# Optimization experiments

Measured on AMD Instinct MI355X. Metric: run time of the kernel, lower is better.

Reference implementation:

```python
import jax, jax.numpy as jnp
import numpy as np

P, F, FR = 288, 7, 12      # time slots per day, days per week, sampling frequency scale
CHEB_K = 2
HID = 64


def _ste(time_index, SE, W_se, b_se, T_tod, T_dow):
    """Spatio-temporal embedding: learned spatial embedding projected to et_dim,
    plus time-of-day and day-of-week temporal embeddings. -> [B, N, et]"""
    t = time_index * FR
    tod = T_tod[t % P]                 # [B, et]
    dow = T_dow[(t // P) % F]          # [B, et]
    se = SE @ W_se + b_se              # [N, et]
    return se[None, :, :] + (tod + dow)[:, None, :]


def _avwgcn(x, STE, R, SC, Wpool, bpool):
    """Adaptive-vertex-weight graph conv (AGCRN-style) with dynamic STE-driven
    adjacency blended with dynamic relation R and static correlation SC.
    x: [B,N,Cin], STE: [B,N,et], R: [B,N,N], SC: [N,N]."""
    A = jax.nn.softmax(
        jax.nn.relu(jnp.einsum('bnd,bmd->bnm', STE, STE)) + R + SC[None], axis=-1)
    # Chebyshev polynomial supports applied to x (T0 = I handled implicitly)
    xs = [x, jnp.einsum('bnm,bmc->bnc', A, x)]
    for _ in range(CHEB_K - 2):
        xs.append(2.0 * jnp.einsum('bnm,bmc->bnc', A, xs[-1]) - xs[-2])
    x_g = jnp.stack(xs, axis=2)                        # [B,N,K,Cin]
    # per-node adaptive weights: W_n = STE @ Wpool; contracted without
    # materializing the [B,N,K,Cin,Cout] tensor
    g = jnp.einsum('bnki,dkio->bndo', x_g, Wpool)      # [B,N,et,Cout]
    out = jnp.einsum('bndo,bnd->bno', g, STE) + jnp.einsum('bnd,do->bno', STE, bpool)
    return out


def setup_inputs() -> dict:
    key = jax.random.key(0)
    ks = jax.random.split(key, 12)
    B, N, Din, et, es = 32, 1024, 1, 16, 16
    std = 0.1
    return {
        "x": jax.random.normal(ks[0], (B, N, Din), jnp.float32),
        "R": jax.random.normal(ks[1], (B, N, N), jnp.float32) * std,
        "state": jax.random.normal(ks[2], (B, N, HID), jnp.float32),
        "SC": jax.random.normal(ks[3], (N, N), jnp.float32) * std,
        "SE": jax.random.normal(ks[4], (N, es), jnp.float32),
        "W_se": jax.random.normal(ks[5], (es, et), jnp.float32) * std,
        "b_se": jnp.zeros((et,), jnp.float32),
        "T_tod": jax.random.normal(ks[6], (P, et), jnp.float32) * std,
        "T_dow": jax.random.normal(ks[7], (F, et), jnp.float32) * std,
        "W_gate": jax.random.normal(ks[8], (et, CHEB_K, Din + HID, 2 * HID), jnp.float32) * std,
        "b_gate": jnp.zeros((et, 2 * HID), jnp.float32),
        "W_upd": jax.random.normal(ks[9], (et, CHEB_K, Din + HID, HID), jnp.float32) * std,
        "b_upd": jnp.zeros((et, HID), jnp.float32),
        "time_index": jax.random.randint(ks[10], (B,), 0, P * F),
    }


def reference(x, R, state, SC, SE, W_se, b_se, T_tod, T_dow,
              W_gate, b_gate, W_upd, b_upd, time_index):
    STE = _ste(time_index, SE, W_se, b_se, T_tod, T_dow)       # [B,N,et]
    ins = jnp.concatenate([x, state], axis=-1)                 # [B,N,Din+H]
    z_r = jax.nn.sigmoid(_avwgcn(ins, STE, R, SC, W_gate, b_gate))
    z, r = jnp.split(z_r, 2, axis=-1)                          # each [B,N,H]
    cand = jnp.concatenate([x, z * state], axis=-1)
    hc = jnp.tanh(_avwgcn(cand, STE, R, SC, W_upd, b_upd))
    return r * state + (1.0 - r) * hc                          # [B,N,H]
```

## Files before the change

kernel.cpp:

```cpp
#include <hip/hip_runtime.h>
#include <math.h>

namespace {
constexpr int BB = 32;
constexpr int NN = 1024;
constexpr int ET = 16;
constexpr int HH = 64;
constexpr int CIN = 65;
constexpr int KI = 2*CIN;
constexpr int COG = 2*HH;
constexpr int COU = HH;
constexpr int PP = 288;
constexpr int FF = 7;
constexpr int FRQ = 12;
constexpr int XK = 160;
constexpr int KP = 168;

typedef __attribute__((ext_vector_type(4))) float f32x4;
typedef __attribute__((ext_vector_type(8))) short s16x8;
typedef unsigned long long ull;

__device__ __forceinline__ float bf2f(unsigned short u) {
    unsigned v = ((unsigned)u) << 16;
    return __builtin_bit_cast(float, v);
}
__device__ __forceinline__ unsigned short f2bf(float f) {
    unsigned u = __builtin_bit_cast(unsigned, f);
    u += 0x7fffu + ((u >> 16) & 1u);
    return (unsigned short)(u >> 16);
}

__global__ void k_prep1(const float* __restrict__ SE, const float* __restrict__ Wse,
                        const float* __restrict__ bse, const float* __restrict__ Ttod,
                        const float* __restrict__ Tdow, const int* __restrict__ tidx,
                        float* __restrict__ se, float* __restrict__ tt) {
    int idx = blockIdx.x*blockDim.x + threadIdx.x;
    if (idx < NN*ET) {
        int n = idx / ET, d = idx % ET;
        float acc = bse[d];
        #pragma unroll
        for (int e = 0; e < ET; ++e) acc += SE[n*ET + e]*Wse[e*ET + d];
        se[idx] = acc;
    } else if (idx < NN*ET + BB*ET) {
        int r = idx - NN*ET;
        int b = r / ET, d = r % ET;
        int t = tidx[b]*FRQ;
        tt[r] = Ttod[(t % PP)*ET + d] + Tdow[((t/PP) % FF)*ET + d];
    }
}

__global__ void k_prep2bf(const float* __restrict__ se, const float* __restrict__ tt,
                          unsigned short* __restrict__ stebf) {
    int idx = blockIdx.x*blockDim.x + threadIdx.x;
    if (idx >= BB*NN*ET) return;
    int d = idx % ET;
    int n = (idx/ET) % NN;
    int b = idx/(ET*NN);
    stebf[idx] = f2bf(se[n*ET+d] + tt[b*ET+d]);
}

__global__ void k_prep3bt(const float* __restrict__ tt, const float* __restrict__ Wg,
                          const float* __restrict__ Wu,
                          unsigned short* __restrict__ Wbtg, unsigned short* __restrict__ Wbtu) {
    int idx = blockIdx.x*blockDim.x + threadIdx.x;
    constexpr int NG = BB*KP*COG;
    constexpr int NU = BB*KP*COU;
    if (idx < NG) {
        int b = idx/(KP*COG); int r = idx%(KP*COG); int ki = r/COG; int o = r%COG;
        float v = 0.f;
        if (ki < KI) {
            #pragma unroll
            for (int d = 0; d < ET; ++d) v += tt[b*ET+d]*Wg[(d*KI + ki)*COG + o];
        }
        Wbtg[((size_t)b*COG + o)*KP + ki] = f2bf(v);
    } else if (idx < NG + NU) {
        int j = idx - NG;
        int b = j/(KP*COU); int r = j%(KP*COU); int ki = r/COU; int o = r%COU;
        float v = 0.f;
        if (ki < KI) {
            #pragma unroll
            for (int d = 0; d < ET; ++d) v += tt[b*ET+d]*Wu[(d*KI + ki)*COU + o];
        }
        Wbtu[((size_t)b*COU + o)*KP + ki] = f2bf(v);
    }
}

__global__ void k_pack(const float* __restrict__ x, const float* __restrict__ sv,
                       const float* __restrict__ axx, const float* __restrict__ ax2,
                       unsigned short* __restrict__ xgbf) {
    int idx = blockIdx.x*blockDim.x + threadIdx.x;
    if (idx >= BB*NN*(XK/2)) return;
    int row = idx/(XK/2), c = idx%(XK/2);
    float v[2];
    #pragma unroll
    for (int h = 0; h < 2; ++h) {
        int k = 2*c + h;
        float val;
        if (k == 0) val = x[row];
        else if (k < CIN) val = sv[(size_t)row*HH + k - 1];
        else if (k == CIN) val = axx[row];
        else if (k < KI) val = ax2[(size_t)row*HH + k - CIN - 1];
        else val = 0.f;
        v[h] = val;
    }
    ((unsigned*)xgbf)[idx] = ((unsigned)f2bf(v[1]) << 16) | f2bf(v[0]);
}

__global__ void k_cvtVt(const float* __restrict__ V, unsigned short* __restrict__ vt) {
    int idx = blockIdx.x*blockDim.x + threadIdx.x;
    if (idx >= BB*128*64) return;
    int och = idx & 63, mb = (idx >> 6) & 127, b = idx >> 13;
    const float* src = V + ((size_t)b*NN + mb*8)*HH + och;
    float v0=src[0], v1=src[HH], v2=src[2*HH], v3=src[3*HH];
    float v4=src[4*HH], v5=src[5*HH], v6=src[6*HH], v7=src[7*HH];
    ull lo = (ull)f2bf(v0) | ((ull)f2bf(v1)<<16) | ((ull)f2bf(v2)<<32) | ((ull)f2bf(v3)<<48);
    ull hi = (ull)f2bf(v4) | ((ull)f2bf(v5)<<16) | ((ull)f2bf(v6)<<32) | ((ull)f2bf(v7)<<48);
    ull* dst = (ull*)(vt + (size_t)idx*8);
    dst[0] = lo; dst[1] = hi;
}

constexpr int SSTR   = 1048;
constexpr int S_OFF  = 0;
constexpr int XV_OFF = 33536;
constexpr int MSH_OFF  = 37632;
constexpr int MSHC_OFF = 37888;
constexpr int LP_OFF   = 37952;
constexpr int AXP_OFF  = 38208;
constexpr int LSH_OFF  = 38464;
constexpr int SMEM_BYTES = 38528;

template<int PASS>
__global__ __launch_bounds__(256, 4) void k_attn(
    const unsigned short* __restrict__ stebf, const float* __restrict__ Rg,
    const float* __restrict__ SCg, const float* __restrict__ xg,
    const unsigned short* __restrict__ vt,
    float* __restrict__ Mr, float* __restrict__ Li, float* __restrict__ Axx,
    float* __restrict__ outp)
{
    extern __shared__ char smem[];
    const int t = threadIdx.x, lane = t & 63, w = t >> 6;
    const int c15 = lane & 15, g = lane >> 4;
    const int strip = blockIdx.x, b = blockIdx.y;
    const size_t bN = (size_t)b * NN;
    const int r0 = strip * 16;

    float* Mshf  = (float*)(smem + MSH_OFF);
    float* MshCf = (float*)(smem + MSHC_OFF);
    float* Lpf   = (float*)(smem + LP_OFF);
    float* Axpf  = (float*)(smem + AXP_OFF);
    float* Lshf  = (float*)(smem + LSH_OFF);

    if (PASS == 1) {
        ((float4*)(smem + XV_OFF))[t] = ((const float4*)(xg + bN))[t];
    }

    {
        s16x8 af = {0,0,0,0,0,0,0,0};
        if (g < 2) af = *(const s16x8*)(stebf + (bN + r0 + c15)*ET + g*8);
        const float* Rb  = Rg  + (bN + r0 + g*4)*NN;
        const float* SCb = SCg + (size_t)(r0 + g*4)*NN;
        float mx0 = -INFINITY, mx1 = -INFINITY, mx2 = -INFINITY, mx3 = -INFINITY;
        float rc[4], scv[4];
        {
            int col = w*16 + c15;
            #pragma unroll
            for (int q = 0; q < 4; ++q) { rc[q] = Rb[(size_t)q*NN + col]; scv[q] = SCb[(size_t)q*NN + col]; }
        }
        for (int j = 0; j < 16; ++j) {
            int colB = j*64 + w*16 + c15;
            s16x8 bf = {0,0,0,0,0,0,0,0};
            if (g < 2) bf = *(const s16x8*)(stebf + (bN + colB)*ET + g*8);
            float rn[4] = {0.f,0.f,0.f,0.f}, sn[4] = {0.f,0.f,0.f,0.f};
            if (j < 15) {
                int col = colB + 64;
                #pragma unroll
                for (int q = 0; q < 4; ++q) { rn[q] = Rb[(size_t)q*NN + col]; sn[q] = SCb[(size_t)q*NN + col]; }
            }
            f32x4 zero = {0.f,0.f,0.f,0.f};
            f32x4 d = __builtin_amdgcn_mfma_f32_16x16x32_bf16(af, bf, zero, 0, 0, 0);
            #pragma unroll
            for (int q = 0; q < 4; ++q) {
                float s = fmaxf(d[q], 0.f) + rc[q] + scv[q];
                if (PASS == 1) {
                    if (q == 0) mx0 = fmaxf(mx0, s);
                    if (q == 1) mx1 = fmaxf(mx1, s);
                    if (q == 2) mx2 = fmaxf(mx2, s);
                    if (q == 3) mx3 = fmaxf(mx3, s);
                }
                int rowl = g*4 + q;
                *(unsigned short*)(smem + S_OFF + (unsigned)(rowl*SSTR + colB)*2u) = f2bf(s);
            }
            #pragma unroll
            for (int q = 0; q < 4; ++q) { rc[q] = rn[q]; scv[q] = sn[q]; }
        }
        if (PASS == 1) {
            float mxa[4] = {mx0, mx1, mx2, mx3};
            #pragma unroll
            for (int q = 0; q < 4; ++q) {
                float m = mxa[q];
                m = fmaxf(m, __shfl_xor(m, 1));
                m = fmaxf(m, __shfl_xor(m, 2));
                m = fmaxf(m, __shfl_xor(m, 4));
                m = fmaxf(m, __shfl_xor(m, 8));
                if (c15 == 0) Mshf[w*16 + g*4 + q] = m;
            }
        }
    }
    __syncthreads();

    if (PASS == 1) {
        if (t < 16) {
            float m = fmaxf(fmaxf(Mshf[t], Mshf[16+t]), fmaxf(Mshf[32+t], Mshf[48+t]));
            MshCf[t] = m;
            Mr[bN + r0 + t] = m;
        }
    } else {
        if (t < 16) MshCf[t] = Mr[bN + r0 + t];
        if (t >= 64 && t < 80) Lshf[t-64] = Li[bN + r0 + (t-64)];
    }
    __syncthreads();

    {
        const int rowl = c15;
        const float m = MshCf[rowl];
        float L = 0.f, ax = 0.f;
        for (int it = 0; it < 16; ++it) {
            int k = w*256 + it*16 + g*4;
            unsigned byteo = (unsigned)(rowl*SSTR + k)*2u;
            ull v = *(ull*)(smem + S_OFF + byteo);
            float s0 = bf2f((unsigned short)v);
            float s1 = bf2f((unsigned short)(v >> 16));
            float s2 = bf2f((unsigned short)(v >> 32));
            float s3 = bf2f((unsigned short)(v >> 48));
            float p0 = __expf(s0 - m), p1 = __expf(s1 - m);
            float p2 = __expf(s2 - m), p3 = __expf(s3 - m);
            if (PASS == 1) {
                float4 xq = *(const float4*)(smem + XV_OFF + k*4);
                L += (p0 + p1) + (p2 + p3);
                ax += p0*xq.x + p1*xq.y + p2*xq.z + p3*xq.w;
            }
            unsigned lo = ((unsigned)f2bf(p1) << 16) | f2bf(p0);
            unsigned hi = ((unsigned)f2bf(p3) << 16) | f2bf(p2);
            *(ull*)(smem + S_OFF + byteo) = ((ull)hi << 32) | lo;
        }
        if (PASS == 1) {
            L += __shfl_xor(L, 16); L += __shfl_xor(L, 32);
            ax += __shfl_xor(ax, 16); ax += __shfl_xor(ax, 32);
            if (g == 0) { Lpf[w*16 + rowl] = L; Axpf[w*16 + rowl] = ax; }
        }
    }
    __syncthreads();
    if (PASS == 1) {
        if (t < 16) {
            float Lt = Lpf[t] + Lpf[16+t] + Lpf[32+t] + Lpf[48+t];
            float li = 1.f / Lt;
            Lshf[t] = li;
            Li[bN + r0 + t] = li;
            Axx[bN + r0 + t] = (Axpf[t] + Axpf[16+t] + Axpf[32+t] + Axpf[48+t]) * li;
        }
        __syncthreads();
    }

    {
        f32x4 acc = {0.f,0.f,0.f,0.f};
        const unsigned short* vtb = vt + ((size_t)b*128*64 + (w*16 + c15))*8;
        #pragma unroll 4
        for (int j = 0; j < 16; ++j) {
            #pragma unroll
            for (int ks = 0; ks < 2; ++ks) {
                s16x8 a  = *(const s16x8*)(smem + S_OFF + (unsigned)(c15*SSTR + j*64 + ks*32 + g*8)*2u);
                s16x8 bv = *(const s16x8*)(vtb + (size_t)(j*8 + ks*4 + g)*512);
                acc = __builtin_amdgcn_mfma_f32_16x16x32_bf16(a, bv, acc, 0, 0, 0);
            }
        }
        #pragma unroll
        for (int q = 0; q < 4; ++q) {
            int rowl = g*4 + q;
            float li = Lshf[rowl];
            outp[(bN + r0 + rowl)*HH + w*16 + c15] = acc[q] * li;
        }
    }
}

template<int COUT>
__global__ __launch_bounds__(256, 2) void k_bapplyM(
    const unsigned short* __restrict__ Wbt, const float* __restrict__ bias,
    const float* __restrict__ tt, const unsigned short* __restrict__ xgbf,
    float* __restrict__ partial)
{
    constexpr int NTP = COUT/64;
    __shared__ __align__(16) unsigned short Wl[COUT*KP];
    const int t = threadIdx.x, lane = t & 63, w = t >> 6;
    const int c15 = lane & 15, g = lane >> 4;
    const int b = blockIdx.y, n0 = blockIdx.x*64;

    {
        const unsigned* src = (const unsigned*)(Wbt + (size_t)b*COUT*KP);
        unsigned* dst = (unsigned*)Wl;
        #pragma unroll
        for (int e = t; e < COUT*KP/2; e += 256) dst[e] = src[e];
    }
    __syncthreads();

    f32x4 acc[4][NTP];
    #pragma unroll
    for (int mt = 0; mt < 4; ++mt)
        #pragma unroll
        for (int nt = 0; nt < NTP; ++nt) acc[mt][nt] = (f32x4){0.f,0.f,0.f,0.f};

    for (int ks = 0; ks < 5; ++ks) {
        s16x8 a[4];
        #pragma unroll
        for (int mt = 0; mt < 4; ++mt)
            a[mt] = *(const s16x8*)(xgbf + ((size_t)b*NN + n0 + mt*16 + c15)*XK + ks*32 + g*8);
        #pragma unroll
        for (int nt = 0; nt < NTP; ++nt) {
            int o = (w*NTP + nt)*16 + c15;
            s16x8 bf = *(const s16x8*)(Wl + o*KP + ks*32 + g*8);
            #pragma unroll
            for (int mt = 0; mt < 4; ++mt)
                acc[mt][nt] = __builtin_amdgcn_mfma_f32_16x16x32_bf16(a[mt], bf, acc[mt][nt], 0, 0, 0);
        }
    }

    #pragma unroll
    for (int nt = 0; nt < NTP; ++nt) {
        int o = (w*NTP + nt)*16 + c15;
        float bo = 0.f;
        #pragma unroll
        for (int d = 0; d < ET; ++d) bo += tt[b*ET+d]*bias[d*COUT+o];
        #pragma unroll
        for (int mt = 0; mt < 4; ++mt)
            #pragma unroll
            for (int q = 0; q < 4; ++q)
                partial[((size_t)b*NN + n0 + mt*16 + g*4 + q)*COUT + o] = acc[mt][nt][q] + bo;
    }
}

__global__ __launch_bounds__(256, 2) void k_napplyM_gate(
    const float* __restrict__ se_g, const float* __restrict__ Wg,
    const float* __restrict__ bias, const unsigned short* __restrict__ xgbf,
    const float* __restrict__ partial, const float* __restrict__ state,
    float* __restrict__ zs, float* __restrict__ rout)
{
    __shared__ __align__(16) unsigned short Wnt[COG*KP];
    __shared__ float se_l[ET];
    const int t = threadIdx.x, lane = t & 63, w = t >> 6;
    const int c15 = lane & 15, g = lane >> 4;
    const int n = blockIdx.x;
    if (t < ET) se_l[t] = se_g[n*ET + t];
    __syncthreads();

    for (int e = t; e < COG*KP; e += 256) {
        int ki = e/COG, o = e%COG;
        float v = 0.f;
        if (ki < KI) {
            #pragma unroll
            for (int d = 0; d < ET; ++d) v += se_l[d]*Wg[(d*KI + ki)*COG + o];
        }
        Wnt[o*KP + ki] = f2bf(v);
    }
    __syncthreads();

    f32x4 acc[2][2];
    #pragma unroll
    for (int mt = 0; mt < 2; ++mt)
        #pragma unroll
        for (int nt = 0; nt < 2; ++nt) acc[mt][nt] = (f32x4){0.f,0.f,0.f,0.f};

    for (int ks = 0; ks < 5; ++ks) {
        s16x8 a[2];
        #pragma unroll
        for (int mt = 0; mt < 2; ++mt)
            a[mt] = *(const s16x8*)(xgbf + ((size_t)(mt*16 + c15)*NN + n)*XK + ks*32 + g*8);
        #pragma unroll
        for (int nt = 0; nt < 2; ++nt) {
            int o = (w*2 + nt)*16 + c15;
            s16x8 bf = *(const s16x8*)(Wnt + o*KP + ks*32 + g*8);
            #pragma unroll
            for (int mt = 0; mt < 2; ++mt)
                acc[mt][nt] = __builtin_amdgcn_mfma_f32_16x16x32_bf16(a[mt], bf, acc[mt][nt], 0, 0, 0);
        }
    }

    #pragma unroll
    for (int nt = 0; nt < 2; ++nt) {
        int o = (w*2 + nt)*16 + c15;
        float bo = 0.f;
        #pragma unroll
        for (int d = 0; d < ET; ++d) bo += se_l[d]*bias[d*COG + o];
        #pragma unroll
        for (int mt = 0; mt < 2; ++mt)
            #pragma unroll
            for (int q = 0; q < 4; ++q) {
                int b = mt*16 + g*4 + q;
                size_t bn = (size_t)b*NN + n;
                float v = acc[mt][nt][q] + bo + partial[bn*COG + o];
                float gv = 1.f/(1.f + __expf(-v));
                if (o < HH) zs[bn*HH + o] = gv * state[bn*HH + o];
                else rout[bn*HH + o - HH] = gv;
            }
    }
}

__global__ __launch_bounds__(256, 2) void k_napplyM_upd(
    const float* __restrict__ se_g, const float* __restrict__ Wu,
    const float* __restrict__ bias, const unsigned short* __restrict__ xgbf,
    const float* __restrict__ partial, const float* __restrict__ rin,
    const float* __restrict__ state, float* __restrict__ out)
{
    __shared__ __align__(16) unsigned short Wnt[COU*KP];
    __shared__ float se_l[ET];
    const int t = threadIdx.x, lane = t & 63, w = t >> 6;
    const int c15 = lane & 15, g = lane >> 4;
    const int n = blockIdx.x;
    if (t < ET) se_l[t] = se_g[n*ET + t];
    __syncthreads();

    for (int e = t; e < COU*KP; e += 256) {
        int ki = e/COU, o = e%COU;
        float v = 0.f;
        if (ki < KI) {
            #pragma unroll
            for (int d = 0; d < ET; ++d) v += se_l[d]*Wu[(d*KI + ki)*COU + o];
        }
        Wnt[o*KP + ki] = f2bf(v);
    }
    __syncthreads();

    f32x4 acc[2];
    acc[0] = (f32x4){0.f,0.f,0.f,0.f};
    acc[1] = (f32x4){0.f,0.f,0.f,0.f};

    for (int ks = 0; ks < 5; ++ks) {
        s16x8 a[2];
        #pragma unroll
        for (int mt = 0; mt < 2; ++mt)
            a[mt] = *(const s16x8*)(xgbf + ((size_t)(mt*16 + c15)*NN + n)*XK + ks*32 + g*8);
        int o = w*16 + c15;
        s16x8 bf = *(const s16x8*)(Wnt + o*KP + ks*32 + g*8);
        #pragma unroll
        for (int mt = 0; mt < 2; ++mt)
            acc[mt] = __builtin_amdgcn_mfma_f32_16x16x32_bf16(a[mt], bf, acc[mt], 0, 0, 0);
    }

    {
        int o = w*16 + c15;
        float bo = 0.f;
        #pragma unroll
        for (int d = 0; d < ET; ++d) bo += se_l[d]*bias[d*COU + o];
        #pragma unroll
        for (int mt = 0; mt < 2; ++mt)
            #pragma unroll
            for (int q = 0; q < 4; ++q) {
                int b = mt*16 + g*4 + q;
                size_t bn = (size_t)b*NN + n;
                float v = acc[mt][q] + bo + partial[bn*COU + o];
                float hc = tanhf(v);
                float rv = rin[bn*HH + o];
                out[bn*HH + o] = rv*state[bn*HH + o] + (1.f - rv)*hc;
            }
    }
}

}

extern "C" void kernel_launch(void* const* d_in, const int* in_sizes, int n_in,
                              void* d_out, int out_size, void* d_ws, size_t ws_size,
                              hipStream_t stream) {
    const float* x     = (const float*)d_in[0];
    const float* R     = (const float*)d_in[1];
    const float* state = (const float*)d_in[2];
    const float* SC    = (const float*)d_in[3];
    const float* SE    = (const float*)d_in[4];
    const float* W_se  = (const float*)d_in[5];
    const float* b_se  = (const float*)d_in[6];
    const float* T_tod = (const float*)d_in[7];
    const float* T_dow = (const float*)d_in[8];
    const float* W_g   = (const float*)d_in[9];
    const float* b_g   = (const float*)d_in[10];
    const float* W_u   = (const float*)d_in[11];
    const float* b_u   = (const float*)d_in[12];
    const int*   tidx  = (const int*)d_in[13];
    float* out = (float*)d_out;
    float* ws = (float*)d_ws;

    float* se    = ws;
    float* tt    = se + 16384;
    float* Mr    = tt + 512;
    float* Li    = Mr + 32768;
    float* axx   = Li + 32768;
    float* axgs  = axx + 32768;
    float* zs    = axgs + 2097152;
    float* rr    = zs + 2097152;
    float* pg    = rr + 2097152;
    unsigned short* stebf = (unsigned short*)(pg + 4194304);
    unsigned short* Wbtg  = stebf + 524288;
    unsigned short* Wbtu  = Wbtg + 688128;
    unsigned short* xgbf  = Wbtu + 344064;
    unsigned short* vt    = xgbf + 5242880;
    float* axcs = axgs;
    float* pu   = pg;

    k_prep1<<<66, 256, 0, stream>>>(SE, W_se, b_se, T_tod, T_dow, tidx, se, tt);
    k_prep2bf<<<2048, 256, 0, stream>>>(se, tt, stebf);
    k_prep3bt<<<4032, 256, 0, stream>>>(tt, W_g, W_u, Wbtg, Wbtu);

    k_cvtVt<<<1024, 256, 0, stream>>>(state, vt);
    k_attn<1><<<dim3(64, 32), 256, SMEM_BYTES, stream>>>(
        stebf, R, SC, x, vt, Mr, Li, axx, axgs);
    k_pack<<<10240, 256, 0, stream>>>(x, state, axx, axgs, xgbf);
    k_bapplyM<COG><<<dim3(16, 32), 256, 0, stream>>>(Wbtg, b_g, tt, xgbf, pg);
    k_napplyM_gate<<<1024, 256, 0, stream>>>(se, W_g, b_g, xgbf, pg, state, zs, rr);

    k_cvtVt<<<1024, 256, 0, stream>>>(zs, vt);
    k_attn<2><<<dim3(64, 32), 256, SMEM_BYTES, stream>>>(
        stebf, R, SC, x, vt, Mr, Li, axx, axcs);
    k_pack<<<10240, 256, 0, stream>>>(x, zs, axx, axcs, xgbf);
    k_bapplyM<COU><<<dim3(16, 32), 256, 0, stream>>>(Wbtu, b_u, tt, xgbf, pu);
    k_napplyM_upd<<<1024, 256, 0, stream>>>(se, W_u, b_u, xgbf, pu, rr, state, out);
}
```

Measured before the change: 268.2 us.

## Contract adaptive weights per embedding dim in one MFMA apply kernel

Replaces the split batch-term/node-term apply kernels (which rebuilt per-node weight matrices in shared memory for every node) with a single kernel. It computes x_g·Wpool[d] for all 16 embedding dims via MFMA and contracts with the full STE in the epilogue. The attention kernel now writes its aggregated outputs directly as bf16 into the packed xg buffer, and gate outputs z*state and r are stored in bf16, removing the separate fp32 intermediates and pack copies. In exchange it does 16× more MFMA work per output, keeps 32 accumulators per lane (register pressure), and adds bf16 rounding to STE in the epilogue and to intermediate activations.

```diff
diff --git a/kernel.cpp b/kernel.cpp
--- a/kernel.cpp
+++ b/kernel.cpp
@@ -14,7 +14,6 @@
 constexpr int FF = 7;
 constexpr int FRQ = 12;
 constexpr int XK = 160;
-constexpr int KP = 168;
 
 typedef __attribute__((ext_vector_type(4))) float f32x4;
 typedef __attribute__((ext_vector_type(8))) short s16x8;
@@ -29,6 +28,8 @@
     u += 0x7fffu + ((u >> 16) & 1u);
     return (unsigned short)(u >> 16);
 }
+__device__ __forceinline__ float ldany(const float* p) { return *p; }
+__device__ __forceinline__ float ldany(const unsigned short* p) { return bf2f(*p); }
 
 __global__ void k_prep1(const float* __restrict__ SE, const float* __restrict__ Wse,
                         const float* __restrict__ bse, const float* __restrict__ Ttod,
@@ -59,60 +60,49 @@
     stebf[idx] = f2bf(se[n*ET+d] + tt[b*ET+d]);
 }
 
-__global__ void k_prep3bt(const float* __restrict__ tt, const float* __restrict__ Wg,
-                          const float* __restrict__ Wu,
-                          unsigned short* __restrict__ Wbtg, unsigned short* __restrict__ Wbtu) {
-    int idx = blockIdx.x*blockDim.x + threadIdx.x;
-    constexpr int NG = BB*KP*COG;
-    constexpr int NU = BB*KP*COU;
-    if (idx < NG) {
-        int b = idx/(KP*COG); int r = idx%(KP*COG); int ki = r/COG; int o = r%COG;
-        float v = 0.f;
-        if (ki < KI) {
-            #pragma unroll
-            for (int d = 0; d < ET; ++d) v += tt[b*ET+d]*Wg[(d*KI + ki)*COG + o];
-        }
-        Wbtg[((size_t)b*COG + o)*KP + ki] = f2bf(v);
-    } else if (idx < NG + NU) {
-        int j = idx - NG;
-        int b = j/(KP*COU); int r = j%(KP*COU); int ki = r/COU; int o = r%COU;
-        float v = 0.f;
-        if (ki < KI) {
-            #pragma unroll
-            for (int d = 0; d < ET; ++d) v += tt[b*ET+d]*Wu[(d*KI + ki)*COU + o];
-        }
-        Wbtu[((size_t)b*COU + o)*KP + ki] = f2bf(v);
-    }
-}
-
-__global__ void k_pack(const float* __restrict__ x, const float* __restrict__ sv,
-                       const float* __restrict__ axx, const float* __restrict__ ax2,
+__global__ void k_prepWpt(const float* __restrict__ Wg, const float* __restrict__ Wu,
+                          unsigned short* __restrict__ Wptg, unsigned short* __restrict__ Wptu) {
+    int idx = blockIdx.x*blockDim.x + threadIdx.x;
+    constexpr int NG2 = ET*COG*XK;
+    constexpr int NU2 = ET*COU*XK;
+    if (idx < NG2) {
+        int d = idx/(COG*XK), r = idx%(COG*XK), o = r/XK, ki = r%XK;
+        float v = (ki < KI) ? Wg[((size_t)d*KI + ki)*COG + o] : 0.f;
+        Wptg[((size_t)d*COG + o)*XK + ki] = f2bf(v);
+    } else if (idx < NG2 + NU2) {
+        int j = idx - NG2;
+        int d = j/(COU*XK), r = j%(COU*XK), o = r/XK, ki = r%XK;
+        float v = (ki < KI) ? Wu[((size_t)d*KI + ki)*COU + o] : 0.f;
+        Wptu[((size_t)d*COU + o)*XK + ki] = f2bf(v);
+    }
+}
+
+template<typename T>
+__global__ void k_pack(const float* __restrict__ x, const T* __restrict__ sv,
                        unsigned short* __restrict__ xgbf) {
     int idx = blockIdx.x*blockDim.x + threadIdx.x;
     if (idx >= BB*NN*(XK/2)) return;
     int row = idx/(XK/2), c = idx%(XK/2);
-    float v[2];
-    #pragma unroll
-    for (int h = 0; h < 2; ++h) {
-        int k = 2*c + h;
-        float val;
-        if (k == 0) val = x[row];
-        else if (k < CIN) val = sv[(size_t)row*HH + k - 1];
-        else if (k == CIN) val = axx[row];
-        else if (k < KI) val = ax2[(size_t)row*HH + k - CIN - 1];
-        else val = 0.f;
-        v[h] = val;
-    }
-    ((unsigned*)xgbf)[idx] = ((unsigned)f2bf(v[1]) << 16) | f2bf(v[0]);
-}
-
-__global__ void k_cvtVt(const float* __restrict__ V, unsigned short* __restrict__ vt) {
+    if (c < 32) {
+        int k0 = 2*c;
+        float v0 = (k0 == 0) ? x[row] : ldany(sv + (size_t)row*HH + k0 - 1);
+        float v1 = ldany(sv + (size_t)row*HH + k0);
+        ((unsigned*)xgbf)[(size_t)row*(XK/2) + c] = ((unsigned)f2bf(v1) << 16) | f2bf(v0);
+    } else if (c == 32) {
+        xgbf[(size_t)row*XK + 64] = f2bf(ldany(sv + (size_t)row*HH + 63));
+    } else if (c >= 65) {
+        ((unsigned*)xgbf)[(size_t)row*(XK/2) + c] = 0;
+    }
+}
+
+template<typename T>
+__global__ void k_cvtVt(const T* __restrict__ V, unsigned short* __restrict__ vt) {
     int idx = blockIdx.x*blockDim.x + threadIdx.x;
     if (idx >= BB*128*64) return;
     int och = idx & 63, mb = (idx >> 6) & 127, b = idx >> 13;
-    const float* src = V + ((size_t)b*NN + mb*8)*HH + och;
-    float v0=src[0], v1=src[HH], v2=src[2*HH], v3=src[3*HH];
-    float v4=src[4*HH], v5=src[5*HH], v6=src[6*HH], v7=src[7*HH];
+    const T* src = V + ((size_t)b*NN + mb*8)*HH + och;
+    float v0=ldany(src), v1=ldany(src+HH), v2=ldany(src+2*HH), v3=ldany(src+3*HH);
+    float v4=ldany(src+4*HH), v5=ldany(src+5*HH), v6=ldany(src+6*HH), v7=ldany(src+7*HH);
     ull lo = (ull)f2bf(v0) | ((ull)f2bf(v1)<<16) | ((ull)f2bf(v2)<<32) | ((ull)f2bf(v3)<<48);
     ull hi = (ull)f2bf(v4) | ((ull)f2bf(v5)<<16) | ((ull)f2bf(v6)<<32) | ((ull)f2bf(v7)<<48);
     ull* dst = (ull*)(vt + (size_t)idx*8);
@@ -134,8 +124,8 @@
     const unsigned short* __restrict__ stebf, const float* __restrict__ Rg,
     const float* __restrict__ SCg, const float* __restrict__ xg,
     const unsigned short* __restrict__ vt,
-    float* __restrict__ Mr, float* __restrict__ Li, float* __restrict__ Axx,
-    float* __restrict__ outp)
+    float* __restrict__ Mr, float* __restrict__ Li,
+    unsigned short* __restrict__ xgout)
 {
     extern __shared__ char smem[];
     const int t = threadIdx.x, lane = t & 63, w = t >> 6;
@@ -256,7 +246,8 @@
             float li = 1.f / Lt;
             Lshf[t] = li;
             Li[bN + r0 + t] = li;
-            Axx[bN + r0 + t] = (Axpf[t] + Axpf[16+t] + Axpf[32+t] + Axpf[48+t]) * li;
+            xgout[(bN + r0 + t)*XK + 65] =
+                f2bf((Axpf[t] + Axpf[16+t] + Axpf[32+t] + Axpf[48+t]) * li);
         }
         __syncthreads();
     }
@@ -277,189 +268,79 @@
         for (int q = 0; q < 4; ++q) {
             int rowl = g*4 + q;
             float li = Lshf[rowl];
-            outp[(bN + r0 + rowl)*HH + w*16 + c15] = acc[q] * li;
-        }
-    }
-}
-
-template<int COUT>
-__global__ __launch_bounds__(256, 2) void k_bapplyM(
-    const unsigned short* __restrict__ Wbt, const float* __restrict__ bias,
-    const float* __restrict__ tt, const unsigned short* __restrict__ xgbf,
-    float* __restrict__ partial)
+            xgout[(bN + r0 + rowl)*XK + 66 + w*16 + c15] = f2bf(acc[q] * li);
+        }
+    }
+}
+
+template<int COUT, int EPI>
+__global__ __launch_bounds__(256, 2) void k_apply(
+    const unsigned short* __restrict__ Wpt, const float* __restrict__ bias,
+    const unsigned short* __restrict__ stebf, const unsigned short* __restrict__ xgbf,
+    const float* __restrict__ state, unsigned short* __restrict__ zsbf,
+    unsigned short* __restrict__ rrbf, float* __restrict__ out)
 {
-    constexpr int NTP = COUT/64;
-    __shared__ __align__(16) unsigned short Wl[COUT*KP];
     const int t = threadIdx.x, lane = t & 63, w = t >> 6;
     const int c15 = lane & 15, g = lane >> 4;
-    const int b = blockIdx.y, n0 = blockIdx.x*64;
-
-    {
-        const unsigned* src = (const unsigned*)(Wbt + (size_t)b*COUT*KP);
-        unsigned* dst = (unsigned*)Wl;
+    const int n0 = blockIdx.x*32, b = blockIdx.y, oh = blockIdx.z;
+    const int o = oh*64 + w*16 + c15;
+
+    f32x4 acc[16][2];
+    #pragma unroll
+    for (int d = 0; d < 16; ++d) {
+        acc[d][0] = (f32x4){0.f,0.f,0.f,0.f};
+        acc[d][1] = (f32x4){0.f,0.f,0.f,0.f};
+    }
+
+    const unsigned short* Ar0 = xgbf + ((size_t)b*NN + n0 + c15)*XK + g*8;
+    const unsigned short* Ar1 = Ar0 + (size_t)16*XK;
+    const unsigned short* Bp  = Wpt + (size_t)o*XK + g*8;
+
+    for (int ks = 0; ks < 5; ++ks) {
+        s16x8 a0 = *(const s16x8*)(Ar0 + ks*32);
+        s16x8 a1 = *(const s16x8*)(Ar1 + ks*32);
         #pragma unroll
-        for (int e = t; e < COUT*KP/2; e += 256) dst[e] = src[e];
-    }
-    __syncthreads();
-
-    f32x4 acc[4][NTP];
+        for (int d = 0; d < 16; ++d) {
+            s16x8 bf = *(const s16x8*)(Bp + (size_t)d*COUT*XK + ks*32);
+            acc[d][0] = __builtin_amdgcn_mfma_f32_16x16x32_bf16(a0, bf, acc[d][0], 0, 0, 0);
+            acc[d][1] = __builtin_amdgcn_mfma_f32_16x16x32_bf16(a1, bf, acc[d][1], 0, 0, 0);
+        }
+    }
+
+    float biasv[16];
     #pragma unroll
-    for (int mt = 0; mt < 4; ++mt)
+    for (int d = 0; d < 16; ++d) biasv[d] = bias[d*COUT + o];
+
+    #pragma unroll
+    for (int mt = 0; mt < 2; ++mt) {
         #pragma unroll
-        for (int nt = 0; nt < NTP; ++nt) acc[mt][nt] = (f32x4){0.f,0.f,0.f,0.f};
-
-    for (int ks = 0; ks < 5; ++ks) {
-        s16x8 a[4];
-        #pragma unroll
-        for (int mt = 0; mt < 4; ++mt)
-            a[mt] = *(const s16x8*)(xgbf + ((size_t)b*NN + n0 + mt*16 + c15)*XK + ks*32 + g*8);
-        #pragma unroll
-        for (int nt = 0; nt < NTP; ++nt) {
-            int o = (w*NTP + nt)*16 + c15;
-            s16x8 bf = *(const s16x8*)(Wl + o*KP + ks*32 + g*8);
-            #pragma unroll
-            for (int mt = 0; mt < 4; ++mt)
-                acc[mt][nt] = __builtin_amdgcn_mfma_f32_16x16x32_bf16(a[mt], bf, acc[mt][nt], 0, 0, 0);
-        }
-    }
-
-    #pragma unroll
-    for (int nt = 0; nt < NTP; ++nt) {
-        int o = (w*NTP + nt)*16 + c15;
-        float bo = 0.f;
-        #pragma unroll
-        for (int d = 0; d < ET; ++d) bo += tt[b*ET+d]*bias[d*COUT+o];
-        #pragma unroll
-        for (int mt = 0; mt < 4; ++mt)
-            #pragma unroll
-            for (int q = 0; q < 4; ++q)
-                partial[((size_t)b*NN + n0 + mt*16 + g*4 + q)*COUT + o] = acc[mt][nt][q] + bo;
-    }
-}
-
-__global__ __launch_bounds__(256, 2) void k_napplyM_gate(
-    const float* __restrict__ se_g, const float* __restrict__ Wg,
-    const float* __restrict__ bias, const unsigned short* __restrict__ xgbf,
-    const float* __restrict__ partial, const float* __restrict__ state,
-    float* __restrict__ zs, float* __restrict__ rout)
-{
-    __shared__ __align__(16) unsigned short Wnt[COG*KP];
-    __shared__ float se_l[ET];
-    const int t = threadIdx.x, lane = t & 63, w = t >> 6;
-    const int c15 = lane & 15, g = lane >> 4;
-    const int n = blockIdx.x;
-    if (t < ET) se_l[t] = se_g[n*ET + t];
-    __syncthreads();
-
-    for (int e = t; e < COG*KP; e += 256) {
-        int ki = e/COG, o = e%COG;
-        float v = 0.f;
-        if (ki < KI) {
-            #pragma unroll
-            for (int d = 0; d < ET; ++d) v += se_l[d]*Wg[(d*KI + ki)*COG + o];
-        }
-        Wnt[o*KP + ki] = f2bf(v);
-    }
-    __syncthreads();
-
-    f32x4 acc[2][2];
-    #pragma unroll
-    for (int mt = 0; mt < 2; ++mt)
-        #pragma unroll
-        for (int nt = 0; nt < 2; ++nt) acc[mt][nt] = (f32x4){0.f,0.f,0.f,0.f};
-
-    for (int ks = 0; ks < 5; ++ks) {
-        s16x8 a[2];
-        #pragma unroll
-        for (int mt = 0; mt < 2; ++mt)
-            a[mt] = *(const s16x8*)(xgbf + ((size_t)(mt*16 + c15)*NN + n)*XK + ks*32 + g*8);
-        #pragma unroll
-        for (int nt = 0; nt < 2; ++nt) {
-            int o = (w*2 + nt)*16 + c15;
-            s16x8 bf = *(const s16x8*)(Wnt + o*KP + ks*32 + g*8);
-            #pragma unroll
-            for (int mt = 0; mt < 2; ++mt)
-                acc[mt][nt] = __builtin_amdgcn_mfma_f32_16x16x32_bf16(a[mt], bf, acc[mt][nt], 0, 0, 0);
-        }
-    }
-
-    #pragma unroll
-    for (int nt = 0; nt < 2; ++nt) {
-        int o = (w*2 + nt)*16 + c15;
-        float bo = 0.f;
-        #pragma unroll
-        for (int d = 0; d < ET; ++d) bo += se_l[d]*bias[d*COG + o];
-        #pragma unroll
-        for (int mt = 0; mt < 2; ++mt)
-            #pragma unroll
-            for (int q = 0; q < 4; ++q) {
-                int b = mt*16 + g*4 + q;
-                size_t bn = (size_t)b*NN + n;
-                float v = acc[mt][nt][q] + bo + partial[bn*COG + o];
-                float gv = 1.f/(1.f + __expf(-v));
-                if (o < HH) zs[bn*HH + o] = gv * state[bn*HH + o];
-                else rout[bn*HH + o - HH] = gv;
-            }
-    }
-}
-
-__global__ __launch_bounds__(256, 2) void k_napplyM_upd(
-    const float* __restrict__ se_g, const float* __restrict__ Wu,
-    const float* __restrict__ bias, const unsigned short* __restrict__ xgbf,
-    const float* __restrict__ partial, const float* __restrict__ rin,
-    const float* __restrict__ state, float* __restrict__ out)
-{
-    __shared__ __align__(16) unsigned short Wnt[COU*KP];
-    __shared__ float se_l[ET];
-    const int t = threadIdx.x, lane = t & 63, w = t >> 6;
-    const int c15 = lane & 15, g = lane >> 4;
-    const int n = blockIdx.x;
-    if (t < ET) se_l[t] = se_g[n*ET + t];
-    __syncthreads();
-
-    for (int e = t; e < COU*KP; e += 256) {
-        int ki = e/COU, o = e%COU;
-        float v = 0.f;
-        if (ki < KI) {
-            #pragma unroll
-            for (int d = 0; d < ET; ++d) v += se_l[d]*Wu[(d*KI + ki)*COU + o];
-        }
-        Wnt[o*KP + ki] = f2bf(v);
-    }
-    __syncthreads();
-
-    f32x4 acc[2];
-    acc[0] = (f32x4){0.f,0.f,0.f,0.f};
-    acc[1] = (f32x4){0.f,0.f,0.f,0.f};
-
-    for (int ks = 0; ks < 5; ++ks) {
-        s16x8 a[2];
-        #pragma unroll
-        for (int mt = 0; mt < 2; ++mt)
-            a[mt] = *(const s16x8*)(xgbf + ((size_t)(mt*16 + c15)*NN + n)*XK + ks*32 + g*8);
-        int o = w*16 + c15;
-        s16x8 bf = *(const s16x8*)(Wnt + o*KP + ks*32 + g*8);
-        #pragma unroll
-        for (int mt = 0; mt < 2; ++mt)
-            acc[mt] = __builtin_amdgcn_mfma_f32_16x16x32_bf16(a[mt], bf, acc[mt], 0, 0, 0);
-    }
-
-    {
-        int o = w*16 + c15;
-        float bo = 0.f;
-        #pragma unroll
-        for (int d = 0; d < ET; ++d) bo += se_l[d]*bias[d*COU + o];
-        #pragma unroll
-        for (int mt = 0; mt < 2; ++mt)
-            #pragma unroll
-            for (int q = 0; q < 4; ++q) {
-                int b = mt*16 + g*4 + q;
-                size_t bn = (size_t)b*NN + n;
-                float v = acc[mt][q] + bo + partial[bn*COU + o];
-                float hc = tanhf(v);
-                float rv = rin[bn*HH + o];
+        for (int q = 0; q < 4; ++q) {
+            int n = n0 + mt*16 + g*4 + q;
+            size_t bn = (size_t)b*NN + n;
+            const ull* sp = (const ull*)(stebf + bn*ET);
+            float val = 0.f;
+            #pragma unroll
+            for (int dd = 0; dd < 4; ++dd) {
+                ull sv4 = sp[dd];
+                float s0 = bf2f((unsigned short)sv4);
+                float s1 = bf2f((unsigned short)(sv4 >> 16));
+                float s2 = bf2f((unsigned short)(sv4 >> 32));
+                float s3 = bf2f((unsigned short)(sv4 >> 48));
+                val += s0*(acc[dd*4+0][mt][q] + biasv[dd*4+0]);
+                val += s1*(acc[dd*4+1][mt][q] + biasv[dd*4+1]);
+                val += s2*(acc[dd*4+2][mt][q] + biasv[dd*4+2]);
+                val += s3*(acc[dd*4+3][mt][q] + biasv[dd*4+3]);
+            }
+            if (EPI == 0) {
+                float gv = 1.f/(1.f + __expf(-val));
+                if (oh == 0) zsbf[bn*HH + o] = f2bf(gv * state[bn*HH + o]);
+                else         rrbf[bn*HH + (o - 64)] = f2bf(gv);
+            } else {
+                float hc = tanhf(val);
+                float rv = bf2f(rrbf[bn*HH + o]);
                 out[bn*HH + o] = rv*state[bn*HH + o] + (1.f - rv)*hc;
             }
+        }
     }
 }
 
@@ -485,38 +366,33 @@
     float* out = (float*)d_out;
     float* ws = (float*)d_ws;
 
-    float* se    = ws;
-    float* tt    = se + 16384;
-    float* Mr    = tt + 512;
-    float* Li    = Mr + 32768;
-    float* axx   = Li + 32768;
-    float* axgs  = axx + 32768;
-    float* zs    = axgs + 2097152;
-    float* rr    = zs + 2097152;
-    float* pg    = rr + 2097152;
-    unsigned short* stebf = (unsigned short*)(pg + 4194304);
-    unsigned short* Wbtg  = stebf + 524288;
-    unsigned short* Wbtu  = Wbtg + 688128;
-    unsigned short* xgbf  = Wbtu + 344064;
-    unsigned short* vt    = xgbf + 5242880;
-    float* axcs = axgs;
-    float* pu   = pg;
+    float* se = ws;
+    float* tt = se + 16384;
+    float* Mr = tt + 512;
+    float* Li = Mr + 32768;
+    unsigned short* stebf = (unsigned short*)(Li + 32768);
+    unsigned short* xgbf  = stebf + 524288;
+    unsigned short* zsbf  = xgbf + 5242880;
+    unsigned short* rrbf  = zsbf + 2097152;
+    unsigned short* vt    = rrbf + 2097152;
+    unsigned short* Wptg  = vt + 2097152;
+    unsigned short* Wptu  = Wptg + 327680;
 
     k_prep1<<<66, 256, 0, stream>>>(SE, W_se, b_se, T_tod, T_dow, tidx, se, tt);
     k_prep2bf<<<2048, 256, 0, stream>>>(se, tt, stebf);
-    k_prep3bt<<<4032, 256, 0, stream>>>(tt, W_g, W_u, Wbtg, Wbtu);
-
-    k_cvtVt<<<1024, 256, 0, stream>>>(state, vt);
+    k_prepWpt<<<1920, 256, 0, stream>>>(W_g, W_u, Wptg, Wptu);
+
+    k_cvtVt<float><<<1024, 256, 0, stream>>>(state, vt);
     k_attn<1><<<dim3(64, 32), 256, SMEM_BYTES, stream>>>(
-        stebf, R, SC, x, vt, Mr, Li, axx, axgs);
-    k_pack<<<10240, 256, 0, stream>>>(x, state, axx, axgs, xgbf);
-    k_bapplyM<COG><<<dim3(16, 32), 256, 0, stream>>>(Wbtg, b_g, tt, xgbf, pg);
-    k_napplyM_gate<<<1024, 256, 0, stream>>>(se, W_g, b_g, xgbf, pg, state, zs, rr);
-
-    k_cvtVt<<<1024, 256, 0, stream>>>(zs, vt);
+        stebf, R, SC, x, vt, Mr, Li, xgbf);
+    k_pack<float><<<10240, 256, 0, stream>>>(x, state, xgbf);
+    k_apply<COG, 0><<<dim3(32, 32, 2), 256, 0, stream>>>(
+        Wptg, b_g, stebf, xgbf, state, zsbf, rrbf, nullptr);
+
+    k_cvtVt<unsigned short><<<1024, 256, 0, stream>>>(zsbf, vt);
     k_attn<2><<<dim3(64, 32), 256, SMEM_BYTES, stream>>>(
-        stebf, R, SC, x, vt, Mr, Li, axx, axcs);
-    k_pack<<<10240, 256, 0, stream>>>(x, zs, axx, axcs, xgbf);
-    k_bapplyM<COU><<<dim3(16, 32), 256, 0, stream>>>(Wbtu, b_u, tt, xgbf, pu);
-    k_napplyM_upd<<<1024, 256, 0, stream>>>(se, W_u, b_u, xgbf, pu, rr, state, out);
-}
+        stebf, R, SC, x, vt, Mr, Li, xgbf);
+    k_pack<unsigned short><<<10240, 256, 0, stream>>>(x, zsbf, xgbf);
+    k_apply<COU, 1><<<dim3(32, 32, 1), 256, 0, stream>>>(
+        Wptu, b_u, stebf, xgbf, state, zsbf, rrbf, out);
+}
```

Measured after the change: 229.1 us. 14.6% less time.
